# Performance work log

Measured on AMD Instinct MI355X. Metric: run time of the kernel, lower is better.

Reference implementation:

```python
import jax, jax.numpy as jnp
import numpy as np

B, L, D, H = 4, 2048, 1024, 16
DH = D // H

def setup_inputs() -> dict:
    key = jax.random.key(0)
    ks = jax.random.split(key, 9)
    s = 1.0 / np.sqrt(D)
    x = jax.random.normal(ks[0], (B, L, D), dtype=jnp.float32)
    Wq = jax.random.uniform(ks[1], (D, D), jnp.float32, -s, s)
    bq = jax.random.uniform(ks[2], (D,), jnp.float32, -s, s)
    Wk = jax.random.uniform(ks[3], (D, D), jnp.float32, -s, s)
    bk = jax.random.uniform(ks[4], (D,), jnp.float32, -s, s)
    Wv = jax.random.uniform(ks[5], (D, D), jnp.float32, -s, s)
    bv = jax.random.uniform(ks[6], (D,), jnp.float32, -s, s)
    Wo = jax.random.uniform(ks[7], (D, D), jnp.float32, -s, s)
    bo = jax.random.uniform(ks[8], (D,), jnp.float32, -s, s)
    mask = jnp.tril(jnp.ones((L, L), dtype=jnp.int32))[None, None]  # [1,1,L,L] causal
    return {"x": x, "Wq": Wq, "bq": bq, "Wk": Wk, "bk": bk, "Wv": Wv, "bv": bv,
            "Wo": Wo, "bo": bo, "mask": mask}

def reference(x, Wq, bq, Wk, bk, Wv, bv, Wo, bo, mask):
    # projections (torch Linear: x @ W.T + b; here W stored transposed already as [D,D])
    q = (x @ Wq + bq).reshape(B, L, H, DH).transpose(0, 2, 1, 3)  # [B,H,L,Dh]
    k = (x @ Wk + bk).reshape(B, L, H, DH).transpose(0, 2, 1, 3)
    v = (x @ Wv + bv).reshape(B, L, H, DH).transpose(0, 2, 1, 3)
    scores = jnp.einsum('bhqd,bhkd->bhqk', q, k) / jnp.sqrt(jnp.float32(DH))
    scores = jnp.where(mask == 0, -jnp.inf, scores)
    attn = jax.nn.softmax(scores, axis=-1)
    out = jnp.einsum('bhqk,bhkd->bhqd', attn, v)  # [B,H,L,Dh]
    out = out.transpose(0, 2, 1, 3).reshape(B, L, D)
    return out @ Wo + bo
```

## Files before the change

kernel.cpp:

```cpp
#include <hip/hip_runtime.h>
#include <hip/hip_bf16.h>


typedef __bf16 bf16;
typedef __bf16 bf16x4 __attribute__((ext_vector_type(4)));
typedef __bf16 bf16x8 __attribute__((ext_vector_type(8)));
typedef float f32x4 __attribute__((ext_vector_type(4)));

#define DEV static __device__ __forceinline__

constexpr int B = 4, L = 2048, D = 1024, H = 16, DH = 64;
constexpr int BL = B * L;
constexpr int GM = 8192, GK = 1024;
constexpr int BKg = 64;
constexpr int PST = 72;

typedef __attribute__((address_space(1))) const void* gptr1;
typedef __attribute__((address_space(3))) void* lptr3;

DEV void load_lds16(const bf16* g, bf16* l) {
  __builtin_amdgcn_global_load_lds((gptr1)g, (lptr3)l, 16, 0, 0);
}

DEV f32x4 mfma(bf16x8 a, bf16x8 b, f32x4 c) {
  return __builtin_amdgcn_mfma_f32_16x16x32_bf16(a, b, c, 0, 0, 0);
}

DEV float scrub(float v) { return (v == v) ? v : 0.f; }

__global__ void sniff_k(const unsigned short* __restrict__ xr, int* flag) {
  __shared__ int cnt;
  if (threadIdx.x == 0) cnt = 0;
  __syncthreads();
  int local = 0;
  for (int i = threadIdx.x; i < 4096; i += 64) {
    const unsigned short u = xr[2 * i];
    const int e = (u >> 7) & 0xFF;
    if (e >= 0x70 && e <= 0x85) local++;
  }
  atomicAdd(&cnt, local);
  __syncthreads();
  if (threadIdx.x == 0) *flag = (cnt > 2048) ? 1 : 0;
}

__global__ __launch_bounds__(256) void cvt_x_k(const void* __restrict__ src,
                                               bf16* __restrict__ dst,
                                               const int* __restrict__ flag, int n) {
  const bool isbf = (*flag != 0);
  const int stride = gridDim.x * blockDim.x * 8;
  for (int idx = (blockIdx.x * blockDim.x + threadIdx.x) * 8; idx < n; idx += stride) {
    bf16x8 o;
    if (isbf) {
      bf16x8 v = *(const bf16x8*)((const bf16*)src + idx);
      #pragma unroll
      for (int j = 0; j < 8; ++j) o[j] = (bf16)scrub((float)v[j]);
    } else {
      const float* s = (const float*)src + idx;
      #pragma unroll
      for (int j = 0; j < 8; ++j) o[j] = (bf16)scrub(s[j]);
    }
    *(bf16x8*)&dst[idx] = o;
  }
}

__global__ __launch_bounds__(256) void wtrans_cvt4_k(const void* __restrict__ W0,
                                                     const void* __restrict__ W1,
                                                     const void* __restrict__ W2,
                                                     const void* __restrict__ W3,
                                                     bf16* __restrict__ dstBase,
                                                     const int* __restrict__ flag) {
  __shared__ bf16 t[32][33];
  const bool isbf = (*flag != 0);
  const int z = blockIdx.z;
  const void* src = (z == 0) ? W0 : (z == 1) ? W1 : (z == 2) ? W2 : W3;
  bf16* dst = dstBase + (size_t)z * D * D;
  const int bx = blockIdx.x * 32, by = blockIdx.y * 32;
  const int tx = threadIdx.x & 31, ty = threadIdx.x >> 5;
  for (int i = ty; i < 32; i += 8) {
    const size_t off = (size_t)(by + i) * D + bx + tx;
    const float v = isbf ? (float)((const bf16*)src)[off] : ((const float*)src)[off];
    t[i][tx] = (bf16)scrub(v);
  }
  __syncthreads();
  for (int i = ty; i < 32; i += 8)
    dst[(size_t)(bx + i) * D + by + tx] = t[tx][i];
}

__global__ __launch_bounds__(256) void vtrans_k(const bf16* __restrict__ V,
                                                bf16* __restrict__ VT) {
  __shared__ __align__(16) bf16 t[64 * 72];
  const int l0 = blockIdx.x * 64, bh = blockIdx.y;
  const int b = bh >> 4, h = bh & 15;
  const int tid = threadIdx.x;
  #pragma unroll
  for (int i = 0; i < 2; ++i) {
    const int o = tid * 8 + i * 2048;
    const int lrow = o >> 6, dcol = o & 63;
    *(bf16x8*)&t[lrow * 72 + dcol] =
        *(const bf16x8*)&V[(size_t)(b * L + l0 + lrow) * D + h * 64 + dcol];
  }
  __syncthreads();
  const int d = tid >> 2, lg = (tid & 3) * 16;
  bf16x8 o0, o1;
  #pragma unroll
  for (int j = 0; j < 8; ++j) o0[j] = t[(lg + j) * 72 + d];
  #pragma unroll
  for (int j = 0; j < 8; ++j) o1[j] = t[(lg + 8 + j) * 72 + d];
  bf16* dst = VT + ((size_t)bh * DH + d) * L + l0 + lg;
  *(bf16x8*)dst = o0;
  *(bf16x8*)(dst + 8) = o1;
}

__global__ __launch_bounds__(256) void qkv_gemm_k(const bf16* __restrict__ A,
                                                  const bf16* __restrict__ Bt,
                                                  const void* __restrict__ bq,
                                                  const void* __restrict__ bk,
                                                  const void* __restrict__ bv,
                                                  bf16* __restrict__ Q,
                                                  bf16* __restrict__ Kk,
                                                  bf16* __restrict__ V,
                                                  const int* __restrict__ flag) {
  __shared__ __align__(16) bf16 As[128 * BKg];
  __shared__ __align__(16) bf16 Bs[128 * BKg];
  const bool isbf = (*flag != 0);
  const int m0 = blockIdx.x * 128, n0 = blockIdx.y * 128;
  const int buf = n0 >> 10, nloc = n0 & 1023;
  bf16* Cb = (buf == 0) ? Q : (buf == 1) ? Kk : V;
  const void* bias = (buf == 0) ? bq : (buf == 1) ? bk : bv;
  const float scale = (buf == 0) ? 0.125f : 1.0f;

  const int tid = threadIdx.x, wave = tid >> 6, lane = tid & 63;
  const int wr = wave >> 1, wc = wave & 1;
  const int quad = lane >> 4, l16 = lane & 15;
  const int srow = lane >> 3;
  const int scol = ((lane ^ srow) & 7) * 8;
  const int l7 = l16 & 7;
  const int s0 = ((quad ^ l7) * 8);
  const int s1 = s0 ^ 32;

  f32x4 acc[4][4] = {};

  for (int k0 = 0; k0 < GK; k0 += BKg) {
    for (int c = wave; c < 16; c += 4) {
      load_lds16(A  + (size_t)(m0 + c * 8 + srow) * GK + k0 + scol, &As[c * 512]);
      load_lds16(Bt + (size_t)(n0 + c * 8 + srow) * GK + k0 + scol, &Bs[c * 512]);
    }
    __syncthreads();
    #pragma unroll
    for (int kk = 0; kk < BKg; kk += 32) {
      const int sk = kk ? s1 : s0;
      bf16x8 af[4], bfr[4];
      #pragma unroll
      for (int i = 0; i < 4; ++i)
        af[i] = *(const bf16x8*)&As[(wr * 64 + i * 16 + l16) * BKg + sk];
      #pragma unroll
      for (int i = 0; i < 4; ++i)
        bfr[i] = *(const bf16x8*)&Bs[(wc * 64 + i * 16 + l16) * BKg + sk];
      #pragma unroll
      for (int mi = 0; mi < 4; ++mi)
        #pragma unroll
        for (int ni = 0; ni < 4; ++ni)
          acc[mi][ni] = mfma(af[mi], bfr[ni], acc[mi][ni]);
    }
    __syncthreads();
  }

  #pragma unroll
  for (int ni = 0; ni < 4; ++ni) {
    const int col = nloc + wc * 64 + ni * 16 + l16;
    const float bv2 = isbf ? (float)((const bf16*)bias)[col] : ((const float*)bias)[col];
    #pragma unroll
    for (int mi = 0; mi < 4; ++mi)
      #pragma unroll
      for (int r = 0; r < 4; ++r) {
        const int row = m0 + wr * 64 + mi * 16 + quad * 4 + r;
        Cb[(size_t)row * D + col] = (bf16)((acc[mi][ni][r] + bv2) * scale);
      }
  }
}

__global__ __launch_bounds__(256) void gemm_bt_k(const bf16* __restrict__ A,
                                                 const bf16* __restrict__ Bt,
                                                 const void* __restrict__ bias,
                                                 void* __restrict__ C,
                                                 const int* __restrict__ flag) {
  __shared__ __align__(16) bf16 As[128 * BKg];
  __shared__ __align__(16) bf16 Bs[128 * BKg];
  const bool isbf = (*flag != 0);
  const int m0 = blockIdx.x * 128, n0 = blockIdx.y * 128;
  const int tid = threadIdx.x, wave = tid >> 6, lane = tid & 63;
  const int wr = wave >> 1, wc = wave & 1;
  const int quad = lane >> 4, l16 = lane & 15;
  const int srow = lane >> 3;
  const int scol = ((lane ^ srow) & 7) * 8;
  const int l7 = l16 & 7;
  const int s0 = ((quad ^ l7) * 8);
  const int s1 = s0 ^ 32;

  f32x4 acc[4][4] = {};

  for (int k0 = 0; k0 < GK; k0 += BKg) {
    for (int c = wave; c < 16; c += 4) {
      load_lds16(A  + (size_t)(m0 + c * 8 + srow) * GK + k0 + scol, &As[c * 512]);
      load_lds16(Bt + (size_t)(n0 + c * 8 + srow) * GK + k0 + scol, &Bs[c * 512]);
    }
    __syncthreads();
    #pragma unroll
    for (int kk = 0; kk < BKg; kk += 32) {
      const int sk = kk ? s1 : s0;
      bf16x8 af[4], bfr[4];
      #pragma unroll
      for (int i = 0; i < 4; ++i)
        af[i] = *(const bf16x8*)&As[(wr * 64 + i * 16 + l16) * BKg + sk];
      #pragma unroll
      for (int i = 0; i < 4; ++i)
        bfr[i] = *(const bf16x8*)&Bs[(wc * 64 + i * 16 + l16) * BKg + sk];
      #pragma unroll
      for (int mi = 0; mi < 4; ++mi)
        #pragma unroll
        for (int ni = 0; ni < 4; ++ni)
          acc[mi][ni] = mfma(af[mi], bfr[ni], acc[mi][ni]);
    }
    __syncthreads();
  }

  bf16* Cb = (bf16*)C;
  float* Cf = (float*)C;
  #pragma unroll
  for (int ni = 0; ni < 4; ++ni) {
    const int col = n0 + wc * 64 + ni * 16 + l16;
    const float bv = isbf ? (float)((const bf16*)bias)[col] : ((const float*)bias)[col];
    #pragma unroll
    for (int mi = 0; mi < 4; ++mi)
      #pragma unroll
      for (int r = 0; r < 4; ++r) {
        const int row = m0 + wr * 64 + mi * 16 + quad * 4 + r;
        const float v = acc[mi][ni][r] + bv;
        if (isbf) Cb[(size_t)row * D + col] = (bf16)v;
        else      Cf[(size_t)row * D + col] = v;
      }
  }
}

__global__ __launch_bounds__(256) void attn_k(bf16* QO,
                                              const bf16* __restrict__ K,
                                              const bf16* __restrict__ VT) {
  __shared__ __align__(16) bf16 Ks[64 * DH];
  __shared__ __align__(16) bf16 Vt[DH * 64];
  __shared__ __align__(16) bf16 Ps[4][16 * PST];

  const int bx = blockIdx.x;
  const int qt = (L / 64 - 1) - (bx >> 6);
  const int bh = bx & 63;
  const int b = bh >> 4, h = bh & 15;
  const int tid = threadIdx.x, wave = tid >> 6, lane = tid & 63;
  const int quad = lane >> 4, l16 = lane & 15;
  const int srow = lane >> 3;
  const int scol = ((lane ^ srow) & 7) * 8;
  const int l7 = l16 & 7;
  const int s0 = ((quad ^ l7) * 8);
  const int s1 = s0 ^ 32;

  bf16* Qb = QO + (size_t)b * L * D + h * DH;
  const bf16* Kb = K + (size_t)b * L * D + h * DH;
  const bf16* VTg = VT + (size_t)bh * DH * L;

  const int qrow = qt * 64 + wave * 16 + l16;
  const bf16x8 qf0 = *(const bf16x8*)(Qb + (size_t)qrow * D + quad * 8);
  const bf16x8 qf1 = *(const bf16x8*)(Qb + (size_t)qrow * D + 32 + quad * 8);

  float m_run = -INFINITY, l_run = 0.f;
  f32x4 o_acc[4] = {};

  for (int kt = 0; kt <= qt; ++kt) {
    for (int c = wave; c < 8; c += 4) {
      load_lds16(Kb  + (size_t)(kt * 64 + c * 8 + srow) * D + scol, &Ks[c * 512]);
      load_lds16(VTg + (size_t)(c * 8 + srow) * L + kt * 64 + scol, &Vt[c * 512]);
    }
    __syncthreads();

    f32x4 s[4];
    #pragma unroll
    for (int nb = 0; nb < 4; ++nb) {
      bf16x8 k0 = *(const bf16x8*)&Ks[(nb * 16 + l16) * DH + s0];
      bf16x8 k1 = *(const bf16x8*)&Ks[(nb * 16 + l16) * DH + s1];
      f32x4 a = {};
      a = mfma(k0, qf0, a);
      a = mfma(k1, qf1, a);
      s[nb] = a;
    }

    if (kt == qt) {
      const int qloc = wave * 16 + l16 + (qt - kt) * 64;
      #pragma unroll
      for (int nb = 0; nb < 4; ++nb)
        #pragma unroll
        for (int r = 0; r < 4; ++r)
          if (nb * 16 + quad * 4 + r > qloc) s[nb][r] = -1e30f;
    }

    float mx = -INFINITY;
    #pragma unroll
    for (int nb = 0; nb < 4; ++nb)
      #pragma unroll
      for (int r = 0; r < 4; ++r) mx = fmaxf(mx, s[nb][r]);
    mx = fmaxf(mx, __shfl_xor(mx, 16, 64));
    mx = fmaxf(mx, __shfl_xor(mx, 32, 64));
    const float mn = fmaxf(m_run, mx);
    const float alpha = __expf(m_run - mn);
    m_run = mn;

    bf16* Pw = &Ps[wave][0];
    float sum = 0.f;
    #pragma unroll
    for (int nb = 0; nb < 4; ++nb) {
      bf16x4 pk;
      #pragma unroll
      for (int r = 0; r < 4; ++r) {
        const float p = __expf(s[nb][r] - mn);
        sum += p;
        pk[r] = (bf16)p;
      }
      *(bf16x4*)&Pw[l16 * PST + nb * 16 + quad * 4] = pk;
    }
    sum += __shfl_xor(sum, 16, 64);
    sum += __shfl_xor(sum, 32, 64);
    l_run = l_run * alpha + sum;

    #pragma unroll
    for (int r = 0; r < 4; ++r) {
      const float ar = __shfl(alpha, quad * 4 + r, 64);
      #pragma unroll
      for (int db = 0; db < 4; ++db) o_acc[db][r] *= ar;
    }

    bf16x8 p0 = *(const bf16x8*)&Pw[l16 * PST + quad * 8];
    bf16x8 p1 = *(const bf16x8*)&Pw[l16 * PST + 32 + quad * 8];
    #pragma unroll
    for (int db = 0; db < 4; ++db) {
      bf16x8 v0 = *(const bf16x8*)&Vt[(db * 16 + l16) * 64 + s0];
      bf16x8 v1 = *(const bf16x8*)&Vt[(db * 16 + l16) * 64 + s1];
      o_acc[db] = mfma(p0, v0, o_acc[db]);
      o_acc[db] = mfma(p1, v1, o_acc[db]);
    }
    __syncthreads();
  }

  #pragma unroll
  for (int r = 0; r < 4; ++r) {
    const float lr = __shfl(l_run, quad * 4 + r, 64);
    const float inv = 1.f / lr;
    const int row = qt * 64 + wave * 16 + quad * 4 + r;
    #pragma unroll
    for (int db = 0; db < 4; ++db)
      Qb[(size_t)row * D + db * 16 + l16] = (bf16)(o_acc[db][r] * inv);
  }
}

extern "C" void kernel_launch(void* const* d_in, const int* in_sizes, int n_in,
                              void* d_out, int out_size, void* d_ws, size_t ws_size,
                              hipStream_t stream) {
  const void* x  = d_in[0];
  const void* Wq = d_in[1];
  const void* bq = d_in[2];
  const void* Wk = d_in[3];
  const void* bk = d_in[4];
  const void* Wv = d_in[5];
  const void* bv = d_in[6];
  const void* Wo = d_in[7];
  const void* bo = d_in[8];

  int* flag = (int*)d_ws;
  char* p = (char*)d_ws + 4096;
  bf16* xc  = (bf16*)p;                 p += (size_t)BL * D * 2;
  bf16* WqT = (bf16*)p;                 p += (size_t)D * D * 2;
  bf16* WkT = (bf16*)p;                 p += (size_t)D * D * 2;
  bf16* WvT = (bf16*)p;                 p += (size_t)D * D * 2;
  bf16* WoT = (bf16*)p;                 p += (size_t)D * D * 2;
  bf16* Qb  = (bf16*)p;                 p += (size_t)BL * D * 2;
  bf16* Kb  = (bf16*)p;                 p += (size_t)BL * D * 2;
  bf16* Vb  = (bf16*)p;
  bf16* VTb = xc;

  sniff_k<<<1, 64, 0, stream>>>((const unsigned short*)x, flag);

  cvt_x_k<<<1024, 256, 0, stream>>>(x, xc, flag, BL * D);
  wtrans_cvt4_k<<<dim3(32, 32, 4), 256, 0, stream>>>(Wq, Wk, Wv, Wo, WqT, flag);

  qkv_gemm_k<<<dim3(GM / 128, 3072 / 128), 256, 0, stream>>>(
      xc, WqT, bq, bk, bv, Qb, Kb, Vb, flag);

  vtrans_k<<<dim3(L / 64, B * H), 256, 0, stream>>>(Vb, VTb);

  attn_k<<<dim3((L / 64) * B * H), 256, 0, stream>>>(Qb, Kb, VTb);

  gemm_bt_k<<<dim3(GM / 128, D / 128), 256, 0, stream>>>(Qb, WoT, bo, d_out, flag);
}
```

Before: 289.1 us.

## Use exp2 softmax with lazy rescaling and MFMA row-sum accumulation

Folds log2(e) into the Q projection scale so the attention softmax can use the hardware exp2 directly. The running max is only updated, and the accumulators rescaled, when some row's new max exceeds the old one by more than a threshold, skipping the rescale and shuffles in most iterations. The row-sum reduction is moved onto MFMA by multiplying the bf16 probabilities with a ones vector, which also makes the denominator use the same rounded values as the numerator. The cost is two extra MFMAs per tile and reliance on the threshold bound to keep exponentials from overflowing.

Result: no change. 291.0 us (+0.7%).

```diff
diff --git a/kernel.cpp b/kernel.cpp
--- a/kernel.cpp
+++ b/kernel.cpp
@@ -127,7 +127,7 @@
   const int buf = n0 >> 10, nloc = n0 & 1023;
   bf16* Cb = (buf == 0) ? Q : (buf == 1) ? Kk : V;
   const void* bias = (buf == 0) ? bq : (buf == 1) ? bk : bv;
-  const float scale = (buf == 0) ? 0.125f : 1.0f;
+  const float scale = (buf == 0) ? 0.18033688011111f : 1.0f;
 
   const int tid = threadIdx.x, wave = tid >> 6, lane = tid & 63;
   const int wr = wave >> 1, wc = wave & 1;
@@ -269,8 +269,13 @@
   const bf16x8 qf0 = *(const bf16x8*)(Qb + (size_t)qrow * D + quad * 8);
   const bf16x8 qf1 = *(const bf16x8*)(Qb + (size_t)qrow * D + 32 + quad * 8);
 
-  float m_run = -INFINITY, l_run = 0.f;
+  bf16x8 ones;
+  #pragma unroll
+  for (int j = 0; j < 8; ++j) ones[j] = (bf16)1.0f;
+
+  float m_run = -INFINITY;
   f32x4 o_acc[4] = {};
+  f32x4 o_sum = {};
 
   for (int kt = 0; kt <= qt; ++kt) {
     for (int c = wave; c < 8; c += 4) {
@@ -291,7 +296,7 @@
     }
 
     if (kt == qt) {
-      const int qloc = wave * 16 + l16 + (qt - kt) * 64;
+      const int qloc = wave * 16 + l16;
       #pragma unroll
       for (int nb = 0; nb < 4; ++nb)
         #pragma unroll
@@ -301,41 +306,40 @@
 
     float mx = -INFINITY;
     #pragma unroll
-    for (int nb = 0; nb < 4; ++nb)
-      #pragma unroll
-      for (int r = 0; r < 4; ++r) mx = fmaxf(mx, s[nb][r]);
+    for (int nb = 0; nb < 4; ++nb) {
+      const float a = fmaxf(fmaxf(s[nb][0], s[nb][1]), fmaxf(s[nb][2], s[nb][3]));
+      mx = fmaxf(mx, a);
+    }
     mx = fmaxf(mx, __shfl_xor(mx, 16, 64));
     mx = fmaxf(mx, __shfl_xor(mx, 32, 64));
-    const float mn = fmaxf(m_run, mx);
-    const float alpha = __expf(m_run - mn);
-    m_run = mn;
+
+    if (!__all(mx <= m_run + 8.f)) {
+      const float mn = fmaxf(m_run, mx);
+      const float alpha = __builtin_amdgcn_exp2f(m_run - mn);
+      m_run = mn;
+      #pragma unroll
+      for (int r = 0; r < 4; ++r) {
+        const float ar = __shfl(alpha, quad * 4 + r, 64);
+        o_sum[r] *= ar;
+        #pragma unroll
+        for (int db = 0; db < 4; ++db) o_acc[db][r] *= ar;
+      }
+    }
 
     bf16* Pw = &Ps[wave][0];
-    float sum = 0.f;
     #pragma unroll
     for (int nb = 0; nb < 4; ++nb) {
       bf16x4 pk;
       #pragma unroll
-      for (int r = 0; r < 4; ++r) {
-        const float p = __expf(s[nb][r] - mn);
-        sum += p;
-        pk[r] = (bf16)p;
-      }
+      for (int r = 0; r < 4; ++r)
+        pk[r] = (bf16)__builtin_amdgcn_exp2f(s[nb][r] - m_run);
       *(bf16x4*)&Pw[l16 * PST + nb * 16 + quad * 4] = pk;
-    }
-    sum += __shfl_xor(sum, 16, 64);
-    sum += __shfl_xor(sum, 32, 64);
-    l_run = l_run * alpha + sum;
-
-    #pragma unroll
-    for (int r = 0; r < 4; ++r) {
-      const float ar = __shfl(alpha, quad * 4 + r, 64);
-      #pragma unroll
-      for (int db = 0; db < 4; ++db) o_acc[db][r] *= ar;
     }
 
     bf16x8 p0 = *(const bf16x8*)&Pw[l16 * PST + quad * 8];
     bf16x8 p1 = *(const bf16x8*)&Pw[l16 * PST + 32 + quad * 8];
+    o_sum = mfma(p0, ones, o_sum);
+    o_sum = mfma(p1, ones, o_sum);
     #pragma unroll
     for (int db = 0; db < 4; ++db) {
       bf16x8 v0 = *(const bf16x8*)&Vt[(db * 16 + l16) * 64 + s0];
@@ -348,8 +352,7 @@
 
   #pragma unroll
   for (int r = 0; r < 4; ++r) {
-    const float lr = __shfl(l_run, quad * 4 + r, 64);
-    const float inv = 1.f / lr;
+    const float inv = 1.f / o_sum[r];
     const int row = qt * 64 + wave * 16 + quad * 4 + r;
     #pragma unroll
     for (int db = 0; db < 4; ++db)
```
